# Performance work log

Hardware: AMD Instinct MI355X
Metric: run time of the kernel (lower is better)

## Reference

```python
import jax, jax.numpy as jnp
import numpy as np

D_MODEL = 1024
NUM_HEADS = 16
SCALE = (D_MODEL // NUM_HEADS) ** -0.5


def setup_inputs() -> dict:
    key = jax.random.key(0)
    ks = jax.random.split(key, 9)
    B, S, D = 4, 2048, D_MODEL
    s = 1.0 / np.sqrt(D)
    x = jax.random.normal(ks[0], (B, S, D), dtype=jnp.float32)
    Wq = jax.random.uniform(ks[1], (D, D), jnp.float32, -s, s)
    bq = jax.random.uniform(ks[2], (D,), jnp.float32, -s, s)
    Wk = jax.random.uniform(ks[3], (D, D), jnp.float32, -s, s)
    bk = jax.random.uniform(ks[4], (D,), jnp.float32, -s, s)
    Wv = jax.random.uniform(ks[5], (D, D), jnp.float32, -s, s)
    bv = jax.random.uniform(ks[6], (D,), jnp.float32, -s, s)
    Wo = jax.random.uniform(ks[7], (D, D), jnp.float32, -s, s)
    bo = jax.random.uniform(ks[8], (D,), jnp.float32, -s, s)
    return {"x": x, "Wq": Wq, "bq": bq, "Wk": Wk, "bk": bk,
            "Wv": Wv, "bv": bv, "Wo": Wo, "bo": bo}


def reference(x, Wq, bq, Wk, bk, Wv, bv, Wo, bo):
    # Linear: x @ W.T + b (torch nn.Linear convention)
    Q = jnp.einsum('bsd,ed->bse', x, Wq) + bq
    K = jnp.einsum('bsd,ed->bse', x, Wk) + bk
    V = jnp.einsum('bsd,ed->bse', x, Wv) + bv
    # Single-head full attention over d_model (module does NOT split heads)
    scores = jnp.einsum('bqd,bkd->bqk', Q, K) * SCALE  # [B,S,S]
    attn = jax.nn.softmax(scores, axis=-1)  # dropout is identity at inference
    out = jnp.einsum('bqk,bkd->bqd', attn, V)
    return jnp.einsum('bsd,ed->bse', out, Wo) + bo
```

## Files before the change

### kernel.cpp

```cpp
#include <hip/hip_runtime.h>
#include <hip/hip_bf16.h>


#define TILE 128
#define BK 32
#define BUFE (TILE * BK)

typedef __attribute__((ext_vector_type(8))) short bf16x8;
typedef __attribute__((ext_vector_type(4))) float f32x4;

__device__ __forceinline__ void stage_tiles(
    const __hip_bfloat16* __restrict__ Ab, const __hip_bfloat16* __restrict__ Bb,
    __hip_bfloat16* As, __hip_bfloat16* Bs,
    long rowBase, long colBase, int K, int k0, int tid)
{
  #pragma unroll
  for (int p = 0; p < 2; ++p) {
    int seg = tid + p * 256;
    int r   = seg >> 2;
    int cq  = seg & 3;
    const __hip_bfloat16* ga = Ab + (rowBase + r) * (long)K + k0 + cq * 8;
    __builtin_amdgcn_global_load_lds(
        (const __attribute__((address_space(1))) void*)ga,
        (__attribute__((address_space(3))) void*)(As + seg * 8), 16, 0, 0);
    const __hip_bfloat16* gb = Bb + (colBase + r) * (long)K + k0 + cq * 8;
    __builtin_amdgcn_global_load_lds(
        (const __attribute__((address_space(1))) void*)gb,
        (__attribute__((address_space(3))) void*)(Bs + seg * 8), 16, 0, 0);
  }
}

__device__ __forceinline__ void gemm_core(
    const __hip_bfloat16* __restrict__ Ab, const __hip_bfloat16* __restrict__ Bb,
    __hip_bfloat16* As, __hip_bfloat16* Bs,
    long rowBase, long colBase, int K, int tid, int wr, int wc, int lr, int q,
    f32x4 acc[4][4])
{
  stage_tiles(Ab, Bb, As, Bs, rowBase, colBase, K, 0, tid);
  int buf = 0;
  for (int k0 = 0; k0 < K; k0 += BK, buf ^= 1) {
    __syncthreads();
    if (k0 + BK < K)
      stage_tiles(Ab, Bb, As + (buf ^ 1) * BUFE, Bs + (buf ^ 1) * BUFE,
                  rowBase, colBase, K, k0 + BK, tid);
    const __hip_bfloat16* Ac = As + buf * BUFE;
    const __hip_bfloat16* Bc = Bs + buf * BUFE;
    bf16x8 af[4], bfr[4];
    #pragma unroll
    for (int mi = 0; mi < 4; ++mi)
      af[mi] = *(const bf16x8*)(Ac + (wr + mi * 16 + lr) * BK + q * 8);
    #pragma unroll
    for (int ni = 0; ni < 4; ++ni)
      bfr[ni] = *(const bf16x8*)(Bc + (wc + ni * 16 + lr) * BK + q * 8);
    #pragma unroll
    for (int mi = 0; mi < 4; ++mi)
      #pragma unroll
      for (int ni = 0; ni < 4; ++ni)
        acc[mi][ni] = __builtin_amdgcn_mfma_f32_16x16x32_bf16(
            af[mi], bfr[ni], acc[mi][ni], 0, 0, 0);
  }
}

__global__ __launch_bounds__(256) void gemm_bt(
    const __hip_bfloat16* __restrict__ A,
    const __hip_bfloat16* __restrict__ B,
    void* __restrict__ Cv,
    const float* __restrict__ bias,
    int K, int ldC,
    long sA, long sB, long sC,
    float scale, int mode)
{
  const long z = blockIdx.z;
  __shared__ __hip_bfloat16 As[2 * BUFE];
  __shared__ __hip_bfloat16 Bs[2 * BUFE];
  const int tid  = threadIdx.x;
  const int lane = tid & 63;
  const int wid  = tid >> 6;
  const int wr   = (wid >> 1) * 64;
  const int wc   = (wid & 1) * 64;
  const int lr   = lane & 15;
  const int q    = lane >> 4;
  const long rowBase = (long)blockIdx.x * TILE;
  const long colBase = (long)blockIdx.y * TILE;

  f32x4 acc[4][4] = {};
  gemm_core(A + z * sA, B + z * sB, As, Bs, rowBase, colBase, K,
            tid, wr, wc, lr, q, acc);

  #pragma unroll
  for (int ni = 0; ni < 4; ++ni) {
    long col = colBase + wc + ni * 16 + lr;
    float bv = bias ? bias[col] : 0.0f;
    #pragma unroll
    for (int mi = 0; mi < 4; ++mi) {
      #pragma unroll
      for (int i = 0; i < 4; ++i) {
        long row = rowBase + wr + mi * 16 + q * 4 + i;
        float v = acc[mi][ni][i] * scale + bv;
        if (mode == 0)
          ((__hip_bfloat16*)Cv)[z * sC + row * (long)ldC + col] = __float2bfloat16(v);
        else
          ((float*)Cv)[z * sC + row * (long)ldC + col] = v;
      }
    }
  }
}


__device__ __forceinline__ void stage_half(
    const __hip_bfloat16* __restrict__ g, __hip_bfloat16* lds,
    long rowBase, int ld, int k0, int tid)
{
  #pragma unroll
  for (int j = 0; j < 2; ++j) {
    int idx = tid + j * 512;
    int r   = idx >> 3;
    int cg  = (idx & 7) ^ (r & 7);
    const __hip_bfloat16* src = g + (rowBase + r) * (long)ld + k0 + cg * 8;
    __builtin_amdgcn_global_load_lds(
        (const __attribute__((address_space(1))) void*)src,
        (__attribute__((address_space(3))) void*)(lds + idx * 8), 16, 0, 0);
  }
}

__device__ __forceinline__ bf16x8 frag256(const __hip_bfloat16* half_, int row, int off)
{
  const char* p = (const char*)half_ + row * 128 + (off ^ ((row & 7) << 4));
  return *(const bf16x8*)p;
}

#define WAITV(N) asm volatile("s_waitcnt vmcnt(" #N ")" ::: "memory")
#define BAR __builtin_amdgcn_s_barrier()

#define READ_A(HALF)                                                        \
  _Pragma("unroll")                                                         \
  for (int ks = 0; ks < 2; ++ks)                                            \
    _Pragma("unroll")                                                       \
    for (int mi = 0; mi < 4; ++mi)                                          \
      a[ks * 4 + mi] = frag256(&L[cur][0][HALF][0], wr + mi * 16 + lr, ks * 64 + q16);

#define READ_B(BREG, HALF)                                                  \
  _Pragma("unroll")                                                         \
  for (int ks = 0; ks < 2; ++ks)                                            \
    _Pragma("unroll")                                                       \
    for (int ni = 0; ni < 2; ++ni)                                          \
      BREG[ks * 2 + ni] = frag256(&L[cur][1][HALF][0], wc + ni * 16 + lr, ks * 64 + q16);

#define MMA_QUAD(MOFF, NOFF, BREG)                                          \
  __builtin_amdgcn_s_setprio(1);                                            \
  _Pragma("unroll")                                                         \
  for (int ks = 0; ks < 2; ++ks)                                            \
    _Pragma("unroll")                                                       \
    for (int mi = 0; mi < 4; ++mi)                                          \
      _Pragma("unroll")                                                     \
      for (int ni = 0; ni < 2; ++ni)                                        \
        acc[(MOFF) + mi][(NOFF) + ni] =                                     \
            __builtin_amdgcn_mfma_f32_16x16x32_bf16(                        \
                a[ks * 4 + mi], BREG[ks * 2 + ni],                          \
                acc[(MOFF) + mi][(NOFF) + ni], 0, 0, 0);                    \
  __builtin_amdgcn_s_setprio(0);

__global__ __launch_bounds__(512, 2) void gemm256_bt(
    const __hip_bfloat16* __restrict__ A,
    const __hip_bfloat16* __restrict__ B,
    void* __restrict__ Cv,
    const float* __restrict__ bias,
    int K, int ldA, int ldB, int ldC,
    long sA_, long sB_, long sC_,
    float scale, int mode)
{
  __shared__ __hip_bfloat16 L[2][2][2][128 * 64];

  const int tid  = threadIdx.x;
  const int lane = tid & 63;
  const int wid  = tid >> 6;
  const int wr   = (wid >> 2) * 64;
  const int wc   = (wid & 3) * 32;
  const int lr   = lane & 15;
  const int q    = lane >> 4;
  const int q16  = q * 16;

  const int NX = gridDim.x, NY = gridDim.y;
  const int nwg = NX * NY * (int)gridDim.z;
  int lin = (int)blockIdx.x + NX * ((int)blockIdx.y + NY * (int)blockIdx.z);
  {
    int xcd = lin & 7, off = lin >> 3;
    int q8 = nwg >> 3, r8 = nwg & 7;
    lin = ((xcd < r8) ? xcd * (q8 + 1) : r8 * (q8 + 1) + (xcd - r8) * q8) + off;
  }
  const int bx = lin % NX;
  const int by = (lin / NX) % NY;
  const long z = lin / (NX * NY);

  const long rowBase = (long)bx * 256;
  const long colBase = (long)by * 256;
  const __hip_bfloat16* Ab = A + z * sA_;
  const __hip_bfloat16* Bb = B + z * sB_;

  f32x4 acc[8][4] = {};
  bf16x8 a[8], bA[4], bB[4];
  const int KT = K >> 6;

  {
    const int kk1 = (KT > 1 ? 1 : 0) * 64;
    stage_half(Ab, &L[0][0][0][0], rowBase,       ldA, 0,   tid);
    stage_half(Bb, &L[0][1][0][0], colBase,       ldB, 0,   tid);
    stage_half(Bb, &L[0][1][1][0], colBase + 128, ldB, 0,   tid);
    stage_half(Ab, &L[0][0][1][0], rowBase + 128, ldA, 0,   tid);
    stage_half(Ab, &L[1][0][0][0], rowBase,       ldA, kk1, tid);
    stage_half(Bb, &L[1][1][0][0], colBase,       ldB, kk1, tid);
    WAITV(8);
    BAR;
  }

  for (int kt = 0; kt < KT; ++kt) {
    const int cur = kt & 1, nxt = cur ^ 1;
    const int t1 = kt + 1 < KT ? kt + 1 : KT - 1;
    const int t2 = kt + 2 < KT ? kt + 2 : KT - 1;
    const int k1 = t1 << 6, k2 = t2 << 6;

    stage_half(Bb, &L[nxt][1][1][0], colBase + 128, ldB, k1, tid);
    WAITV(8);
    READ_A(0);
    READ_B(bA, 0);
    BAR;
    MMA_QUAD(0, 0, bA);
    stage_half(Ab, &L[nxt][0][1][0], rowBase + 128, ldA, k1, tid);
    WAITV(8);
    READ_B(bB, 1);
    BAR;
    MMA_QUAD(0, 2, bB);
    stage_half(Ab, &L[cur][0][0][0], rowBase, ldA, k2, tid);
    WAITV(8);
    READ_A(1);
    BAR;
    MMA_QUAD(4, 2, bB);
    stage_half(Bb, &L[cur][1][0][0], colBase, ldB, k2, tid);
    WAITV(8);
    BAR;
    MMA_QUAD(4, 0, bA);
  }
  WAITV(0);

  const long cz = z * sC_;
  #pragma unroll
  for (int n = 0; n < 4; ++n) {
    long col = colBase + (n >> 1) * 128 + wc + (n & 1) * 16 + lr;
    float bv = bias ? bias[col] : 0.0f;
    #pragma unroll
    for (int m = 0; m < 8; ++m) {
      long row0 = rowBase + (m >> 2) * 128 + wr + (m & 3) * 16 + q * 4;
      f32x4 v = acc[m][n];
      #pragma unroll
      for (int i = 0; i < 4; ++i) {
        float val = v[i] * scale + bv;
        if (mode == 0)
          ((__hip_bfloat16*)Cv)[cz + (row0 + i) * (long)ldC + col] =
              __float2bfloat16(val);
        else
          ((float*)Cv)[cz + (row0 + i) * (long)ldC + col] = val;
      }
    }
  }
}

__global__ __launch_bounds__(256) void cvt_f32_bf16(
    const float* __restrict__ in, __hip_bfloat16* __restrict__ out)
{
  long i = ((long)blockIdx.x * 256 + threadIdx.x) * 8;
  float4 a = *(const float4*)(in + i);
  float4 b = *(const float4*)(in + i + 4);
  bf16x8 o;
  o[0] = __builtin_bit_cast(short, __float2bfloat16(a.x));
  o[1] = __builtin_bit_cast(short, __float2bfloat16(a.y));
  o[2] = __builtin_bit_cast(short, __float2bfloat16(a.z));
  o[3] = __builtin_bit_cast(short, __float2bfloat16(a.w));
  o[4] = __builtin_bit_cast(short, __float2bfloat16(b.x));
  o[5] = __builtin_bit_cast(short, __float2bfloat16(b.y));
  o[6] = __builtin_bit_cast(short, __float2bfloat16(b.z));
  o[7] = __builtin_bit_cast(short, __float2bfloat16(b.w));
  *(bf16x8*)(out + i) = o;
}

__global__ __launch_bounds__(256) void cvt_t_f32_bf16(
    const float* __restrict__ in, __hip_bfloat16* __restrict__ out)
{
  __shared__ __hip_bfloat16 t[64][65];
  const int tid = threadIdx.x;
  const long rb = (long)blockIdx.y * 64;
  const long cb = (long)blockIdx.x * 64;
  const int r0 = tid >> 4;
  const int c0 = (tid & 15) * 4;
  #pragma unroll
  for (int p = 0; p < 4; ++p) {
    int r = r0 + p * 16;
    float4 v = *(const float4*)(in + (rb + r) * 1024 + cb + c0);
    t[c0 + 0][r] = __float2bfloat16(v.x);
    t[c0 + 1][r] = __float2bfloat16(v.y);
    t[c0 + 2][r] = __float2bfloat16(v.z);
    t[c0 + 3][r] = __float2bfloat16(v.w);
  }
  __syncthreads();
  #pragma unroll
  for (int p = 0; p < 4; ++p) {
    int r = r0 + p * 16;
    __hip_bfloat16* o = out + (cb + r) * 1024 + rb + c0;
    o[0] = t[r][c0 + 0]; o[1] = t[r][c0 + 1];
    o[2] = t[r][c0 + 2]; o[3] = t[r][c0 + 3];
  }
}

__global__ __launch_bounds__(256) void bias_vo(
    const float* __restrict__ Wo, const float* __restrict__ bv,
    const float* __restrict__ bo, float* __restrict__ bfinal)
{
  int e = blockIdx.x * 4 + (threadIdx.x >> 6);
  int lane = threadIdx.x & 63;
  const float* row = Wo + (long)e * 1024;
  float s = 0.0f;
  #pragma unroll
  for (int p = 0; p < 4; ++p) {
    float4 w = *(const float4*)(row + p * 256 + lane * 4);
    float4 b = *(const float4*)(bv + p * 256 + lane * 4);
    s += w.x * b.x + w.y * b.y + w.z * b.z + w.w * b.w;
  }
  #pragma unroll
  for (int o = 32; o; o >>= 1) s += __shfl_xor(s, o);
  if (lane == 0) bfinal[e] = s + bo[e];
}

__global__ __launch_bounds__(256) void cat_bias(
    const float* __restrict__ a, const float* __restrict__ b,
    float* __restrict__ o)
{
  int i = blockIdx.x * 256 + threadIdx.x;
  o[i] = (i < 1024) ? a[i] : b[i - 1024];
}

__global__ __launch_bounds__(256) void softmax_rows(__hip_bfloat16* __restrict__ P)
{
  const int tid  = threadIdx.x;
  const int lane = tid & 63;
  const int wid  = tid >> 6;
  __hip_bfloat16* p = P + (long)blockIdx.x * 2048 + tid * 8;

  bf16x8 v = *(const bf16x8*)p;
  float x[8];
  #pragma unroll
  for (int i = 0; i < 8; ++i)
    x[i] = __uint_as_float(((unsigned)(unsigned short)v[i]) << 16);

  float m = x[0];
  #pragma unroll
  for (int i = 1; i < 8; ++i) m = fmaxf(m, x[i]);
  #pragma unroll
  for (int o = 32; o; o >>= 1) m = fmaxf(m, __shfl_xor(m, o));

  __shared__ float rmax[4], rsum[4];
  if (lane == 0) rmax[wid] = m;
  __syncthreads();
  m = fmaxf(fmaxf(rmax[0], rmax[1]), fmaxf(rmax[2], rmax[3]));

  float e[8], s = 0.0f;
  #pragma unroll
  for (int i = 0; i < 8; ++i) { e[i] = __expf(x[i] - m); s += e[i]; }
  #pragma unroll
  for (int o = 32; o; o >>= 1) s += __shfl_xor(s, o);
  if (lane == 0) rsum[wid] = s;
  __syncthreads();
  s = (rsum[0] + rsum[1]) + (rsum[2] + rsum[3]);

  float inv = 1.0f / s;
  bf16x8 ov;
  #pragma unroll
  for (int i = 0; i < 8; ++i) {
    __hip_bfloat16 h = __float2bfloat16(e[i] * inv);
    ov[i] = __builtin_bit_cast(short, h);
  }
  *(bf16x8*)p = ov;
}

extern "C" void kernel_launch(void* const* d_in, const int* in_sizes, int n_in,
                              void* d_out, int out_size, void* d_ws, size_t ws_size,
                              hipStream_t stream) {
  const float* x  = (const float*)d_in[0];
  const float* Wq = (const float*)d_in[1];
  const float* bq = (const float*)d_in[2];
  const float* Wk = (const float*)d_in[3];
  const float* bk = (const float*)d_in[4];
  const float* Wv = (const float*)d_in[5];
  const float* bv = (const float*)d_in[6];
  const float* Wo = (const float*)d_in[7];
  const float* bo = (const float*)d_in[8];
  float* out = (float*)d_out;

  const long B = 4, S = 2048, D = 1024;
  char* ws = (char*)d_ws;
  __hip_bfloat16* xb   = (__hip_bfloat16*)ws; ws += B * S * D * 2;
  __hip_bfloat16* Wqkb = (__hip_bfloat16*)ws; ws += 2 * D * D * 2;
  __hip_bfloat16* Wob  = (__hip_bfloat16*)ws; ws += D * D * 2;
  __hip_bfloat16* QK   = (__hip_bfloat16*)ws; ws += (B * S) * (2 * D) * 2;
  __hip_bfloat16* VWot = (__hip_bfloat16*)ws; ws += B * D * S * 2;
  __hip_bfloat16* P    = (__hip_bfloat16*)ws; ws += B * S * S * 2;
  __hip_bfloat16* Wvtb   = QK;
  __hip_bfloat16* Wvo    = P;
  float*          bfinal = (float*)Wob;
  float*          bqk    = (float*)Wob + 1024;

  dim3 blk(256);
  dim3 blk5(512);
  cvt_f32_bf16<<<dim3(4096), blk, 0, stream>>>(x,  xb);
  cvt_f32_bf16<<<dim3(512),  blk, 0, stream>>>(Wq, Wqkb);
  cvt_f32_bf16<<<dim3(512),  blk, 0, stream>>>(Wk, Wqkb + D * D);
  cvt_f32_bf16<<<dim3(512),  blk, 0, stream>>>(Wo, Wob);
  cvt_t_f32_bf16<<<dim3(16, 16), blk, 0, stream>>>(Wv, Wvtb);

  gemm_bt<<<dim3(8, 8, 1), blk, 0, stream>>>(Wob, Wvtb, Wvo,
                                             nullptr, 1024, 1024, 0, 0, 0, 1.0f, 0);
  bias_vo<<<dim3(256), blk, 0, stream>>>(Wo, bv, bo, bfinal);
  cat_bias<<<dim3(8), blk, 0, stream>>>(bq, bk, bqk);

  gemm256_bt<<<dim3(32, 8, 1), blk5, 0, stream>>>(
      xb, Wqkb, QK, bqk, 1024, 1024, 1024, 2048, 0, 0, 0, 1.0f, 0);
  gemm256_bt<<<dim3(4, 8, 4), blk5, 0, stream>>>(
      Wvo, xb, VWot, nullptr, 1024, 1024, 1024, 2048, 0, S * D, D * S, 1.0f, 0);
  gemm256_bt<<<dim3(8, 8, 4), blk5, 0, stream>>>(
      QK, QK + 1024, P, nullptr, 1024, 2048, 2048, 2048,
      S * 2048, S * 2048, S * S, 0.125f, 0);
  softmax_rows<<<dim3(8192), blk, 0, stream>>>(P);
  gemm256_bt<<<dim3(8, 4, 4), blk5, 0, stream>>>(
      P, VWot, out, bfinal, 2048, 2048, 2048, 1024,
      S * S, D * S, S * D, 1.0f, 2);
}
```

Baseline: 306.5 us.

## Restructure 256x256 GEMM main loop into two-stage unrolled ping-pong pipeline

```diff
diff --git a/kernel.cpp b/kernel.cpp
--- a/kernel.cpp
+++ b/kernel.cpp
@@ -106,7 +106,6 @@
   }
 }
 
-
 __device__ __forceinline__ void stage_half(
     const __hip_bfloat16* __restrict__ g, __hip_bfloat16* lds,
     long rowBase, int ld, int k0, int tid)
@@ -130,21 +129,28 @@
 }
 
 #define WAITV(N) asm volatile("s_waitcnt vmcnt(" #N ")" ::: "memory")
+#define LGKM0                                          \
+  do {                                                 \
+    asm volatile("s_waitcnt lgkmcnt(0)" ::: "memory"); \
+    __builtin_amdgcn_sched_barrier(0);                 \
+  } while (0)
 #define BAR __builtin_amdgcn_s_barrier()
 
-#define READ_A(HALF)                                                        \
+#define READ_A8(BUF, HALF)                                                  \
   _Pragma("unroll")                                                         \
   for (int ks = 0; ks < 2; ++ks)                                            \
     _Pragma("unroll")                                                       \
     for (int mi = 0; mi < 4; ++mi)                                          \
-      a[ks * 4 + mi] = frag256(&L[cur][0][HALF][0], wr + mi * 16 + lr, ks * 64 + q16);
-
-#define READ_B(BREG, HALF)                                                  \
+      a[ks * 4 + mi] =                                                      \
+          frag256(&L[BUF][0][HALF][0], wr + mi * 16 + lr, ks * 64 + q16);
+
+#define READ_B4(BREG, BUF, HALF)                                            \
   _Pragma("unroll")                                                         \
   for (int ks = 0; ks < 2; ++ks)                                            \
     _Pragma("unroll")                                                       \
     for (int ni = 0; ni < 2; ++ni)                                          \
-      BREG[ks * 2 + ni] = frag256(&L[cur][1][HALF][0], wc + ni * 16 + lr, ks * 64 + q16);
+      BREG[ks * 2 + ni] =                                                   \
+          frag256(&L[BUF][1][HALF][0], wc + ni * 16 + lr, ks * 64 + q16);
 
 #define MMA_QUAD(MOFF, NOFF, BREG)                                          \
   __builtin_amdgcn_s_setprio(1);                                            \
@@ -199,46 +205,52 @@
 
   f32x4 acc[8][4] = {};
   bf16x8 a[8], bA[4], bB[4];
-  const int KT = K >> 6;
-
-  {
-    const int kk1 = (KT > 1 ? 1 : 0) * 64;
-    stage_half(Ab, &L[0][0][0][0], rowBase,       ldA, 0,   tid);
-    stage_half(Bb, &L[0][1][0][0], colBase,       ldB, 0,   tid);
-    stage_half(Bb, &L[0][1][1][0], colBase + 128, ldB, 0,   tid);
-    stage_half(Ab, &L[0][0][1][0], rowBase + 128, ldA, 0,   tid);
-    stage_half(Ab, &L[1][0][0][0], rowBase,       ldA, kk1, tid);
-    stage_half(Bb, &L[1][1][0][0], colBase,       ldB, kk1, tid);
-    WAITV(8);
-    BAR;
-  }
-
-  for (int kt = 0; kt < KT; ++kt) {
-    const int cur = kt & 1, nxt = cur ^ 1;
-    const int t1 = kt + 1 < KT ? kt + 1 : KT - 1;
-    const int t2 = kt + 2 < KT ? kt + 2 : KT - 1;
-    const int k1 = t1 << 6, k2 = t2 << 6;
-
-    stage_half(Bb, &L[nxt][1][1][0], colBase + 128, ldB, k1, tid);
-    WAITV(8);
-    READ_A(0);
-    READ_B(bA, 0);
-    BAR;
-    MMA_QUAD(0, 0, bA);
-    stage_half(Ab, &L[nxt][0][1][0], rowBase + 128, ldA, k1, tid);
-    WAITV(8);
-    READ_B(bB, 1);
-    BAR;
-    MMA_QUAD(0, 2, bB);
-    stage_half(Ab, &L[cur][0][0][0], rowBase, ldA, k2, tid);
-    WAITV(8);
-    READ_A(1);
-    BAR;
-    MMA_QUAD(4, 2, bB);
-    stage_half(Bb, &L[cur][1][0][0], colBase, ldB, k2, tid);
-    WAITV(8);
-    BAR;
-    MMA_QUAD(4, 0, bA);
+  const int KT  = K >> 6;
+  const int NIT = KT >> 1;
+
+  stage_half(Ab, &L[0][0][0][0], rowBase,       ldA, 0,  tid);
+  stage_half(Bb, &L[0][1][0][0], colBase,       ldB, 0,  tid);
+  stage_half(Bb, &L[0][1][1][0], colBase + 128, ldB, 0,  tid);
+  stage_half(Ab, &L[0][0][1][0], rowBase + 128, ldA, 0,  tid);
+  stage_half(Ab, &L[1][0][0][0], rowBase,       ldA, 64, tid);
+  stage_half(Bb, &L[1][1][0][0], colBase,       ldB, 64, tid);
+  stage_half(Bb, &L[1][1][1][0], colBase + 128, ldB, 64, tid);
+  stage_half(Ab, &L[1][0][1][0], rowBase + 128, ldA, 64, tid);
+  WAITV(12);
+  BAR;
+
+  for (int it = 0; it < NIT; ++it) {
+    const int t2 = 2 * it + 2, t3 = 2 * it + 3;
+    const int k2 = (t2 < KT ? t2 : KT - 1) << 6;
+    const int k3 = (t3 < KT ? t3 : KT - 1) << 6;
+    READ_A8(0, 0); READ_B4(bA, 0, 0);
+    BAR; LGKM0; MMA_QUAD(0, 0, bA);
+    WAITV(10); BAR;
+    stage_half(Ab, &L[0][0][0][0], rowBase, ldA, k2, tid);
+    READ_B4(bB, 0, 1);
+    BAR; LGKM0; MMA_QUAD(0, 2, bB);
+    WAITV(10); BAR;
+    stage_half(Bb, &L[0][1][0][0], colBase, ldB, k2, tid);
+    READ_A8(0, 1);
+    BAR; LGKM0; MMA_QUAD(4, 2, bB); BAR;
+    stage_half(Bb, &L[0][1][1][0], colBase + 128, ldB, k2, tid);
+    BAR; MMA_QUAD(4, 0, bA);
+    WAITV(10); BAR;
+    stage_half(Ab, &L[0][0][1][0], rowBase + 128, ldA, k2, tid);
+    READ_A8(1, 0); READ_B4(bA, 1, 0);
+    BAR; LGKM0; MMA_QUAD(0, 0, bA);
+    WAITV(10); BAR;
+    stage_half(Ab, &L[1][0][0][0], rowBase, ldA, k3, tid);
+    READ_B4(bB, 1, 1);
+    BAR; LGKM0; MMA_QUAD(0, 2, bB);
+    WAITV(10); BAR;
+    stage_half(Bb, &L[1][1][0][0], colBase, ldB, k3, tid);
+    READ_A8(1, 1);
+    BAR; LGKM0; MMA_QUAD(4, 2, bB); BAR;
+    stage_half(Bb, &L[1][1][1][0], colBase + 128, ldB, k3, tid);
+    stage_half(Ab, &L[1][0][1][0], rowBase + 128, ldA, k3, tid);
+    BAR; MMA_QUAD(4, 0, bA);
+    WAITV(12); BAR;
   }
   WAITV(0);
 
```

After: 316.1 us. 3.1% more time.

## Add 128x256 tile GEMM with triple-buffered LDS for small-grid GEMMs

Applied to the files above, without the earlier changes.

```diff
diff --git a/kernel.cpp b/kernel.cpp
--- a/kernel.cpp
+++ b/kernel.cpp
@@ -106,7 +106,6 @@
   }
 }
 
-
 __device__ __forceinline__ void stage_half(
     const __hip_bfloat16* __restrict__ g, __hip_bfloat16* lds,
     long rowBase, int ld, int k0, int tid)
@@ -132,19 +131,34 @@
 #define WAITV(N) asm volatile("s_waitcnt vmcnt(" #N ")" ::: "memory")
 #define BAR __builtin_amdgcn_s_barrier()
 
-#define READ_A(HALF)                                                        \
+__device__ __forceinline__ void xcd_decode(int NX, int NY, int NZ,
+                                           int& bx, int& by, long& z)
+{
+  const int nwg = NX * NY * NZ;
+  int lin = (int)blockIdx.x + NX * ((int)blockIdx.y + NY * (int)blockIdx.z);
+  int xcd = lin & 7, off = lin >> 3;
+  int q8 = nwg >> 3, r8 = nwg & 7;
+  lin = ((xcd < r8) ? xcd * (q8 + 1) : r8 * (q8 + 1) + (xcd - r8) * q8) + off;
+  by = lin % NY;
+  bx = (lin / NY) % NX;
+  z  = lin / (NY * NX);
+}
+
+#define READ_A8(BUF, HALF)                                                  \
   _Pragma("unroll")                                                         \
   for (int ks = 0; ks < 2; ++ks)                                            \
     _Pragma("unroll")                                                       \
     for (int mi = 0; mi < 4; ++mi)                                          \
-      a[ks * 4 + mi] = frag256(&L[cur][0][HALF][0], wr + mi * 16 + lr, ks * 64 + q16);
-
-#define READ_B(BREG, HALF)                                                  \
+      a[ks * 4 + mi] =                                                      \
+          frag256(&L[BUF][0][HALF][0], wr + mi * 16 + lr, ks * 64 + q16);
+
+#define READ_B4(BREG, BUF, HALF)                                            \
   _Pragma("unroll")                                                         \
   for (int ks = 0; ks < 2; ++ks)                                            \
     _Pragma("unroll")                                                       \
     for (int ni = 0; ni < 2; ++ni)                                          \
-      BREG[ks * 2 + ni] = frag256(&L[cur][1][HALF][0], wc + ni * 16 + lr, ks * 64 + q16);
+      BREG[ks * 2 + ni] =                                                   \
+          frag256(&L[BUF][1][HALF][0], wc + ni * 16 + lr, ks * 64 + q16);
 
 #define MMA_QUAD(MOFF, NOFF, BREG)                                          \
   __builtin_amdgcn_s_setprio(1);                                            \
@@ -180,17 +194,8 @@
   const int q    = lane >> 4;
   const int q16  = q * 16;
 
-  const int NX = gridDim.x, NY = gridDim.y;
-  const int nwg = NX * NY * (int)gridDim.z;
-  int lin = (int)blockIdx.x + NX * ((int)blockIdx.y + NY * (int)blockIdx.z);
-  {
-    int xcd = lin & 7, off = lin >> 3;
-    int q8 = nwg >> 3, r8 = nwg & 7;
-    lin = ((xcd < r8) ? xcd * (q8 + 1) : r8 * (q8 + 1) + (xcd - r8) * q8) + off;
-  }
-  const int bx = lin % NX;
-  const int by = (lin / NX) % NY;
-  const long z = lin / (NX * NY);
+  int bx, by; long z;
+  xcd_decode(gridDim.x, gridDim.y, gridDim.z, bx, by, z);
 
   const long rowBase = (long)bx * 256;
   const long colBase = (long)by * 256;
@@ -221,18 +226,18 @@
 
     stage_half(Bb, &L[nxt][1][1][0], colBase + 128, ldB, k1, tid);
     WAITV(8);
-    READ_A(0);
-    READ_B(bA, 0);
+    READ_A8(cur, 0);
+    READ_B4(bA, cur, 0);
     BAR;
     MMA_QUAD(0, 0, bA);
     stage_half(Ab, &L[nxt][0][1][0], rowBase + 128, ldA, k1, tid);
     WAITV(8);
-    READ_B(bB, 1);
+    READ_B4(bB, cur, 1);
     BAR;
     MMA_QUAD(0, 2, bB);
     stage_half(Ab, &L[cur][0][0][0], rowBase, ldA, k2, tid);
     WAITV(8);
-    READ_A(1);
+    READ_A8(cur, 1);
     BAR;
     MMA_QUAD(4, 2, bB);
     stage_half(Bb, &L[cur][1][0][0], colBase, ldB, k2, tid);
@@ -250,6 +255,122 @@
     #pragma unroll
     for (int m = 0; m < 8; ++m) {
       long row0 = rowBase + (m >> 2) * 128 + wr + (m & 3) * 16 + q * 4;
+      f32x4 v = acc[m][n];
+      #pragma unroll
+      for (int i = 0; i < 4; ++i) {
+        float val = v[i] * scale + bv;
+        if (mode == 0)
+          ((__hip_bfloat16*)Cv)[cz + (row0 + i) * (long)ldC + col] =
+              __float2bfloat16(val);
+        else
+          ((float*)Cv)[cz + (row0 + i) * (long)ldC + col] = val;
+      }
+    }
+  }
+}
+
+__global__ __launch_bounds__(512, 2) void gemm128_bt(
+    const __hip_bfloat16* __restrict__ A,
+    const __hip_bfloat16* __restrict__ B,
+    void* __restrict__ Cv,
+    const float* __restrict__ bias,
+    int K, int ldA, int ldB, int ldC,
+    long sA_, long sB_, long sC_,
+    float scale, int mode)
+{
+  __shared__ __hip_bfloat16 L[3][3][128 * 64];
+
+  const int tid  = threadIdx.x;
+  const int lane = tid & 63;
+  const int wid  = tid >> 6;
+  const int wr   = (wid >> 2) * 64;
+  const int wc   = (wid & 3) * 32;
+  const int lr   = lane & 15;
+  const int q    = lane >> 4;
+  const int q16  = q * 16;
+
+  int bx, by; long z;
+  xcd_decode(gridDim.x, gridDim.y, gridDim.z, bx, by, z);
+
+  const long rowBase = (long)bx * 128;
+  const long colBase = (long)by * 256;
+  const __hip_bfloat16* Ab = A + z * sA_;
+  const __hip_bfloat16* Bb = B + z * sB_;
+
+  f32x4 acc[4][4] = {};
+  bf16x8 a[8], bA[4], bB[4];
+  const int KT = K >> 6;
+
+  {
+    const int kk1 = (KT > 1 ? 1 : 0) * 64;
+    stage_half(Ab, &L[0][0][0], rowBase,       ldA, 0,   tid);
+    stage_half(Bb, &L[0][1][0], colBase,       ldB, 0,   tid);
+    stage_half(Bb, &L[0][2][0], colBase + 128, ldB, 0,   tid);
+    stage_half(Ab, &L[1][0][0], rowBase,       ldA, kk1, tid);
+    stage_half(Bb, &L[1][1][0], colBase,       ldB, kk1, tid);
+    stage_half(Bb, &L[1][2][0], colBase + 128, ldB, kk1, tid);
+    WAITV(8);
+    BAR;
+  }
+
+  int cur = 0, nx2 = 2;
+  for (int t = 0; t < KT; ++t) {
+    const int kc = ((t + 2 < KT) ? (t + 2) : (KT - 1)) << 6;
+    stage_half(Ab, &L[nx2][0][0], rowBase,       ldA, kc, tid);
+    stage_half(Bb, &L[nx2][1][0], colBase,       ldB, kc, tid);
+    WAITV(10);
+    #pragma unroll
+    for (int ks = 0; ks < 2; ++ks)
+      #pragma unroll
+      for (int mi = 0; mi < 4; ++mi)
+        a[ks * 4 + mi] = frag256(&L[cur][0][0], wr + mi * 16 + lr, ks * 64 + q16);
+    #pragma unroll
+    for (int ks = 0; ks < 2; ++ks)
+      #pragma unroll
+      for (int ni = 0; ni < 2; ++ni)
+        bA[ks * 2 + ni] = frag256(&L[cur][1][0], wc + ni * 16 + lr, ks * 64 + q16);
+    BAR;
+    __builtin_amdgcn_s_setprio(1);
+    #pragma unroll
+    for (int ks = 0; ks < 2; ++ks)
+      #pragma unroll
+      for (int mi = 0; mi < 4; ++mi)
+        #pragma unroll
+        for (int ni = 0; ni < 2; ++ni)
+          acc[mi][ni] = __builtin_amdgcn_mfma_f32_16x16x32_bf16(
+              a[ks * 4 + mi], bA[ks * 2 + ni], acc[mi][ni], 0, 0, 0);
+    __builtin_amdgcn_s_setprio(0);
+    stage_half(Bb, &L[nx2][2][0], colBase + 128, ldB, kc, tid);
+    WAITV(8);
+    #pragma unroll
+    for (int ks = 0; ks < 2; ++ks)
+      #pragma unroll
+      for (int ni = 0; ni < 2; ++ni)
+        bB[ks * 2 + ni] = frag256(&L[cur][2][0], wc + ni * 16 + lr, ks * 64 + q16);
+    BAR;
+    __builtin_amdgcn_s_setprio(1);
+    #pragma unroll
+    for (int ks = 0; ks < 2; ++ks)
+      #pragma unroll
+      for (int mi = 0; mi < 4; ++mi)
+        #pragma unroll
+        for (int ni = 0; ni < 2; ++ni)
+          acc[mi][2 + ni] = __builtin_amdgcn_mfma_f32_16x16x32_bf16(
+              a[ks * 4 + mi], bB[ks * 2 + ni], acc[mi][2 + ni], 0, 0, 0);
+    __builtin_amdgcn_s_setprio(0);
+    cur = (cur == 2) ? 0 : cur + 1;
+    nx2 = (nx2 == 2) ? 0 : nx2 + 1;
+  }
+  WAITV(0);
+
+  const long cz = z * sC_;
+  #pragma unroll
+  for (int n = 0; n < 4; ++n) {
+    long col = colBase + (n >> 1) * 128 + wc + (n & 1) * 16 + lr;
+    float bv = bias ? bias[col] : 0.0f;
+    #pragma unroll
+    for (int m = 0; m < 4; ++m) {
+      long row0 = rowBase + wr + m * 16 + q * 4;
       f32x4 v = acc[m][n];
       #pragma unroll
       for (int i = 0; i < 4; ++i) {
@@ -422,13 +543,13 @@
 
   gemm256_bt<<<dim3(32, 8, 1), blk5, 0, stream>>>(
       xb, Wqkb, QK, bqk, 1024, 1024, 1024, 2048, 0, 0, 0, 1.0f, 0);
-  gemm256_bt<<<dim3(4, 8, 4), blk5, 0, stream>>>(
+  gemm128_bt<<<dim3(8, 8, 4), blk5, 0, stream>>>(
       Wvo, xb, VWot, nullptr, 1024, 1024, 1024, 2048, 0, S * D, D * S, 1.0f, 0);
   gemm256_bt<<<dim3(8, 8, 4), blk5, 0, stream>>>(
       QK, QK + 1024, P, nullptr, 1024, 2048, 2048, 2048,
       S * 2048, S * 2048, S * S, 0.125f, 0);
   softmax_rows<<<dim3(8192), blk, 0, stream>>>(P);
-  gemm256_bt<<<dim3(8, 4, 4), blk5, 0, stream>>>(
+  gemm128_bt<<<dim3(16, 4, 4), blk5, 0, stream>>>(
       P, VWot, out, bfinal, 2048, 2048, 2048, 1024,
       S * S, D * S, S * D, 1.0f, 2);
 }
```

After: 278.6 us. 9.1% less time.
